# Kernel optimization log

Measured on AMD Instinct MI355X. Metric: run time of the kernel, lower is better.

Reference implementation:

```python
import jax, jax.numpy as jnp
import numpy as np

B, N_E, N_T, N_R, N_W2V = 32, 500000, 2000000, 200, 300


def setup_inputs() -> dict:
    key = jax.random.key(0)
    ks = jax.random.split(key, 11)
    x = jax.random.uniform(ks[0], (B, N_E), dtype=jnp.float32)  # k-hot-like entity vector
    q = jax.random.normal(ks[1], (B, N_W2V), dtype=jnp.float32)
    # Reified KB: one nonzero per row of M_subj / M_rel / M_obj -> index vectors
    subj_idx = jax.random.randint(ks[2], (N_T,), 0, N_E)
    rel_idx = jax.random.randint(ks[3], (N_T,), 0, N_R)
    obj_idx = jax.random.randint(ks[4], (N_T,), 0, N_E)
    s = 1.0 / np.sqrt(N_W2V)
    W1 = jax.random.uniform(ks[5], (N_W2V, N_R), minval=-s, maxval=s, dtype=jnp.float32)
    b1 = jax.random.uniform(ks[6], (N_R,), minval=-s, maxval=s, dtype=jnp.float32)
    W2 = jax.random.uniform(ks[7], (N_W2V, N_R), minval=-s, maxval=s, dtype=jnp.float32)
    b2 = jax.random.uniform(ks[8], (N_R,), minval=-s, maxval=s, dtype=jnp.float32)
    W3 = jax.random.uniform(ks[9], (N_W2V, N_R), minval=-s, maxval=s, dtype=jnp.float32)
    b3 = jax.random.uniform(ks[10], (N_R,), minval=-s, maxval=s, dtype=jnp.float32)
    return {"x": x, "q": q, "subj_idx": subj_idx, "rel_idx": rel_idx,
            "obj_idx": obj_idx, "W1": W1, "b1": b1, "W2": W2, "b2": b2,
            "W3": W3, "b3": b3, "n_hop": 3}


def reference(x, q, subj_idx, rel_idx, obj_idx, W1, b1, W2, b2, W3, b3, n_hop):
    # one follow step: x_t = x @ M_subj.T (gather), r_t = r @ M_rel.T (gather),
    # x_new = (x_t * r_t) @ M_obj (scatter-add over object entities)
    def one_step(x, r):
        m = x[:, subj_idx] * r[:, rel_idx]          # [B, N_T]
        return jnp.zeros_like(x).at[:, obj_idx].add(m)  # [B, N_E]

    if n_hop >= 1:
        x = one_step(x, q @ W1 + b1)
    if n_hop >= 2:
        x = one_step(x, q @ W2 + b2)
    if n_hop >= 3:
        x = one_step(x, q @ W3 + b3)
    return x
```

## Files before the change

### kernel.cpp

```cpp
#include <hip/hip_runtime.h>
#include <hip/hip_fp16.h>

#define B 32
#define NW2V 300
#define NR 200
#define NBLK 256
#define MAXNB 2048
#define CS_THREADS 1024

__global__ void compute_r_kernel(const float* __restrict__ q,
                                 const float* __restrict__ W,
                                 const float* __restrict__ bias,
                                 float* __restrict__ rT) {
    int tid = blockIdx.x * blockDim.x + threadIdx.x;
    if (tid >= NR * B) return;
    int b = tid & (B - 1);
    int j = tid >> 5;
    float acc = bias[j];
    for (int k = 0; k < NW2V; ++k)
        acc += q[b * NW2V + k] * W[k * NR + j];
    rT[j * B + b] = acc;
}

__global__ void transpose_in_kernel(const float* __restrict__ x,
                                    __half* __restrict__ xT, int n_e) {
    __shared__ float tile[64][33];
    int e0 = blockIdx.x * 64;
    for (int p = 0; p < 8; ++p) {
        int idx = p * 256 + threadIdx.x;
        int b = idx >> 6, e = idx & 63;
        if (e0 + e < n_e) tile[e][b] = x[(size_t)b * n_e + e0 + e];
    }
    __syncthreads();
    for (int p = 0; p < 8; ++p) {
        int idx = p * 256 + threadIdx.x;
        int b = idx & 31, e = idx >> 5;
        if (e0 + e < n_e) xT[(size_t)(e0 + e) * B + b] = __float2half(tile[e][b]);
    }
}

__global__ void transpose_out_kernel(const __half* __restrict__ xT,
                                     float* __restrict__ out, int n_e) {
    __shared__ float tile[64][33];
    int e0 = blockIdx.x * 64;
    for (int p = 0; p < 8; ++p) {
        int idx = p * 256 + threadIdx.x;
        int b = idx & 31, e = idx >> 5;
        if (e0 + e < n_e) tile[e][b] = __half2float(xT[(size_t)(e0 + e) * B + b]);
    }
    __syncthreads();
    for (int p = 0; p < 8; ++p) {
        int idx = p * 256 + threadIdx.x;
        int b = idx >> 6, e = idx & 63;
        if (e0 + e < n_e) out[(size_t)b * n_e + e0 + e] = tile[e][b];
    }
}


__global__ void count_kernel(const int* __restrict__ obj,
                             int* __restrict__ hist_bb, int n_t, int nb, int chunk) {
    __shared__ int h[MAXNB];
    for (int i = threadIdx.x; i < nb; i += CS_THREADS) h[i] = 0;
    __syncthreads();
    int t0 = blockIdx.x * chunk;
    int t1 = min(t0 + chunk, n_t);
    for (int t = t0 + threadIdx.x; t < t1; t += CS_THREADS)
        atomicAdd(&h[obj[t] >> 8], 1);
    __syncthreads();
    for (int i = threadIdx.x; i < nb; i += CS_THREADS)
        hist_bb[(size_t)i * NBLK + blockIdx.x] = h[i];
}

__global__ void block_reduce_kernel(const int* __restrict__ vals,
                                    int* __restrict__ blockSums, int len) {
    __shared__ int s[256];
    int i = blockIdx.x * 256 + threadIdx.x;
    s[threadIdx.x] = (i < len) ? vals[i] : 0;
    __syncthreads();
    for (int off = 128; off > 0; off >>= 1) {
        if (threadIdx.x < off) s[threadIdx.x] += s[threadIdx.x + off];
        __syncthreads();
    }
    if (threadIdx.x == 0) blockSums[blockIdx.x] = s[0];
}

__global__ void scan_blocksums_kernel(int* __restrict__ blockSums, int nb) {
    __shared__ int s[256];
    int t = threadIdx.x;
    int local[8];
    int run = 0;
    for (int c = 0; c < 8; ++c) {
        int j = t * 8 + c;
        run += (j < nb) ? blockSums[j] : 0;
        local[c] = run;
    }
    s[t] = run;
    __syncthreads();
    for (int off = 1; off < 256; off <<= 1) {
        int v = (t >= off) ? s[t - off] : 0;
        __syncthreads();
        s[t] += v;
        __syncthreads();
    }
    int threadExcl = s[t] - run;
    for (int c = 0; c < 8; ++c) {
        int j = t * 8 + c;
        if (j < nb) blockSums[j] = threadExcl + (c == 0 ? 0 : local[c - 1]);
    }
}

__global__ void scan_apply_kernel(const int* __restrict__ vals,
                                  const int* __restrict__ blockSums,
                                  int* __restrict__ out, int len) {
    __shared__ int s[256];
    int t = threadIdx.x;
    int i = blockIdx.x * 256 + t;
    int c = (i < len) ? vals[i] : 0;
    s[t] = c;
    __syncthreads();
    for (int off = 1; off < 256; off <<= 1) {
        int v = (t >= off) ? s[t - off] : 0;
        __syncthreads();
        s[t] += v;
        __syncthreads();
    }
    if (i < len) out[i] = blockSums[blockIdx.x] + s[t] - c;
}

__global__ void scatter8_kernel(const int* __restrict__ subj,
                                const int* __restrict__ rel,
                                const int* __restrict__ obj,
                                const int* __restrict__ base_bb,
                                uint2* __restrict__ packed2,
                                int n_t, int nb, int chunk) {
    __shared__ int h[MAXNB];
    __shared__ int sbase[MAXNB];
    for (int i = threadIdx.x; i < nb; i += CS_THREADS) {
        h[i] = 0;
        sbase[i] = base_bb[(size_t)i * NBLK + blockIdx.x];
    }
    __syncthreads();
    int t0 = blockIdx.x * chunk;
    int t1 = min(t0 + chunk, n_t);
    for (int t = t0 + threadIdx.x; t < t1; t += CS_THREADS) {
        int o = obj[t];
        int bin = o >> 8;
        int rank = atomicAdd(&h[bin], 1);
        packed2[sbase[bin] + rank] = make_uint2(
            (unsigned)subj[t] | ((unsigned)rel[t] << 19), (unsigned)o);
    }
}

__global__ void fine_sort_kernel(const uint2* __restrict__ in,
                                 uint2* __restrict__ outp,
                                 const int* __restrict__ base_bb,
                                 int n_t, int nb) {
    __shared__ int cnt[256];
    __shared__ int cur[256];
    int bin = blockIdx.x;
    int beg = base_bb[(size_t)bin * NBLK];
    int end = (bin + 1 < nb) ? base_bb[(size_t)(bin + 1) * NBLK] : n_t;
    int t = threadIdx.x;
    cnt[t] = 0;
    __syncthreads();
    for (int i = beg + t; i < end; i += 256)
        atomicAdd(&cnt[in[i].y & 255], 1);
    __syncthreads();
    int c = cnt[t];
    __syncthreads();
    for (int off = 1; off < 256; off <<= 1) {
        int v = (t >= off) ? cnt[t - off] : 0;
        __syncthreads();
        cnt[t] += v;
        __syncthreads();
    }
    cur[t] = cnt[t] - c + beg;
    __syncthreads();
    for (int i = beg + t; i < end; i += 256) {
        uint2 e = in[i];
        int pos = atomicAdd(&cur[e.y & 255], 1);
        outp[pos] = e;
    }
}

__global__ void hop_merge_kernel(const __half2* __restrict__ xT2,
                                 const float2* __restrict__ rT2,
                                 __half2* __restrict__ outT2,
                                 const uint2* __restrict__ sorted2,
                                 const int* __restrict__ n_hop,
                                 int hop, int n_e, int n_t) {
    int tid = threadIdx.x;
    if (*n_hop < hop) {
        long total = (long)n_e * 16;
        for (long i = (long)blockIdx.x * 256 + tid; i < total;
             i += (long)gridDim.x * 256)
            outT2[i] = xT2[i];
        return;
    }
    __shared__ uint2 ent[256];
    int base = blockIdx.x * 256;
    int cnt = min(256, n_t - base);
    ent[tid] = (tid < cnt) ? sorted2[base + tid]
                           : make_uint2(0u, 0xFFFFFFFFu);
    __syncthreads();
    int g = tid >> 4, l = tid & 15;
    int e0 = g * 16;
    int m = min(16, cnt - e0);
    if (m <= 0) return;

    __half2 xh[16];
#pragma unroll
    for (int j = 0; j < 16; ++j) {
        int s = (int)(ent[e0 + j].x & 0x7FFFF);
        xh[j] = xT2[(size_t)s * 16 + l];
    }

    float a0 = 0.f, a1 = 0.f;
    unsigned cur_o = ent[e0].y;
#pragma unroll
    for (int j = 0; j < 16; ++j) {
        if (j < m) {
            uint2 e = ent[e0 + j];
            float2 rf = rT2[(size_t)(e.x >> 19) * 16 + l];
            float2 xf = __half22float2(xh[j]);
            if (e.y != cur_o) {
                unsafeAtomicAdd(&outT2[(size_t)cur_o * 16 + l],
                                __floats2half2_rn(a0, a1));
                a0 = 0.f; a1 = 0.f;
                cur_o = e.y;
            }
            a0 += xf.x * rf.x;
            a1 += xf.y * rf.y;
        }
    }
    unsafeAtomicAdd(&outT2[(size_t)cur_o * 16 + l], __floats2half2_rn(a0, a1));
}

extern "C" void kernel_launch(void* const* d_in, const int* in_sizes, int n_in,
                              void* d_out, int out_size, void* d_ws, size_t ws_size,
                              hipStream_t stream) {
    const float* x    = (const float*)d_in[0];
    const float* q    = (const float*)d_in[1];
    const int*   subj = (const int*)d_in[2];
    const int*   rel  = (const int*)d_in[3];
    const int*   obj  = (const int*)d_in[4];
    const float* W1   = (const float*)d_in[5];
    const float* bb1  = (const float*)d_in[6];
    const float* W2   = (const float*)d_in[7];
    const float* bb2  = (const float*)d_in[8];
    const float* W3   = (const float*)d_in[9];
    const float* bb3  = (const float*)d_in[10];
    const int*   n_hop = (const int*)d_in[11];
    float* out = (float*)d_out;

    const int n_e   = in_sizes[0] / B;
    const int n_t   = in_sizes[2];
    const int nb    = (n_e + 255) >> 8;
    const int chunk = (n_t + NBLK - 1) / NBLK;
    const int scanLen = nb * NBLK;
    const int snb   = (scanLen + 255) / 256;

    char* w = (char*)d_ws;
    __half* bufA    = (__half*)w;                     w += 32000000;
    __half* bufB    = (__half*)w;                     w += 32000000;
    float*  rT      = (float*)w;                      w += 76800;
    int*    hist_bb = (int*)w;                        w += 2097152;
    int*    base_bb = (int*)w;                        w += 2097152;
    int*    bsums   = (int*)w;                        w += 16384;
    uint2*  packed2 = (uint2*)w;                      w += 16000000;
    uint2*  sorted2 = (uint2*)w;

    const int rblocks = (NR * B + 255) / 256;
    compute_r_kernel<<<rblocks, 256, 0, stream>>>(q, W1, bb1, rT + 0 * NR * B);
    compute_r_kernel<<<rblocks, 256, 0, stream>>>(q, W2, bb2, rT + 1 * NR * B);
    compute_r_kernel<<<rblocks, 256, 0, stream>>>(q, W3, bb3, rT + 2 * NR * B);

    const int tblocks = (n_e + 63) / 64;
    transpose_in_kernel<<<tblocks, 256, 0, stream>>>(x, bufA, n_e);

    count_kernel<<<NBLK, CS_THREADS, 0, stream>>>(obj, hist_bb, n_t, nb, chunk);
    block_reduce_kernel<<<snb, 256, 0, stream>>>(hist_bb, bsums, scanLen);
    scan_blocksums_kernel<<<1, 256, 0, stream>>>(bsums, snb);
    scan_apply_kernel<<<snb, 256, 0, stream>>>(hist_bb, bsums, base_bb, scanLen);
    scatter8_kernel<<<NBLK, CS_THREADS, 0, stream>>>(subj, rel, obj, base_bb,
                                                     packed2, n_t, nb, chunk);
    fine_sort_kernel<<<nb, 256, 0, stream>>>(packed2, sorted2, base_bb, n_t, nb);

    const int hblocks = (n_t + 255) / 256;
    const size_t bytes = (size_t)n_e * B * sizeof(__half);

    hipMemsetAsync(bufB, 0, bytes, stream);
    hop_merge_kernel<<<hblocks, 256, 0, stream>>>((const __half2*)bufA,
        (const float2*)(rT + 0 * NR * B), (__half2*)bufB, sorted2, n_hop, 1, n_e, n_t);
    hipMemsetAsync(bufA, 0, bytes, stream);
    hop_merge_kernel<<<hblocks, 256, 0, stream>>>((const __half2*)bufB,
        (const float2*)(rT + 1 * NR * B), (__half2*)bufA, sorted2, n_hop, 2, n_e, n_t);
    hipMemsetAsync(bufB, 0, bytes, stream);
    hop_merge_kernel<<<hblocks, 256, 0, stream>>>((const __half2*)bufA,
        (const float2*)(rT + 2 * NR * B), (__half2*)bufB, sorted2, n_hop, 3, n_e, n_t);

    transpose_out_kernel<<<tblocks, 256, 0, stream>>>(bufB, out, n_e);
}
```

Measured before the change: 336.4 us.

## Accumulate each object bucket in shared memory instead of global half2 atomics

Each hop kernel now runs one block per 256-entity object bucket. The block walks that bucket's sorted triples and accumulates into an fp32 shared-memory tile with LDS atomics, then writes the tile to the output once. This drops the three hipMemsetAsync zeroing passes and the global half2 atomics, and keeps accumulation in fp32 until the final store. In exchange each block loops serially over its bucket, about 1000 triples, and needs roughly 35KB of LDS per block, which may limit occupancy.

```diff
diff --git a/kernel.cpp b/kernel.cpp
--- a/kernel.cpp
+++ b/kernel.cpp
@@ -183,57 +183,78 @@
     }
 }
 
-__global__ void hop_merge_kernel(const __half2* __restrict__ xT2,
-                                 const float2* __restrict__ rT2,
-                                 __half2* __restrict__ outT2,
-                                 const uint2* __restrict__ sorted2,
-                                 const int* __restrict__ n_hop,
-                                 int hop, int n_e, int n_t) {
+__global__ void hop_bucket_kernel(const __half2* __restrict__ xT2,
+                                  const float2* __restrict__ rT2,
+                                  __half2* __restrict__ outT2,
+                                  const uint2* __restrict__ sorted2,
+                                  const int* __restrict__ base_bb,
+                                  const int* __restrict__ n_hop,
+                                  int hop, int n_e, int n_t, int nb) {
     int tid = threadIdx.x;
+    int bin = blockIdx.x;
+    int eb = bin << 8;
+    int lim = min(256, n_e - eb);
+
     if (*n_hop < hop) {
-        long total = (long)n_e * 16;
-        for (long i = (long)blockIdx.x * 256 + tid; i < total;
-             i += (long)gridDim.x * 256)
-            outT2[i] = xT2[i];
+        for (int p = tid; p < lim * 16; p += 256)
+            outT2[(size_t)eb * 16 + p] = xT2[(size_t)eb * 16 + p];
         return;
     }
+
+    __shared__ float acc[256][33];
     __shared__ uint2 ent[256];
-    int base = blockIdx.x * 256;
-    int cnt = min(256, n_t - base);
-    ent[tid] = (tid < cnt) ? sorted2[base + tid]
-                           : make_uint2(0u, 0xFFFFFFFFu);
-    __syncthreads();
+    float* af = &acc[0][0];
+    for (int i = tid; i < 256 * 33; i += 256) af[i] = 0.f;
+
+    int beg = base_bb[(size_t)bin * NBLK];
+    int end = (bin + 1 < nb) ? base_bb[(size_t)(bin + 1) * NBLK] : n_t;
     int g = tid >> 4, l = tid & 15;
     int e0 = g * 16;
-    int m = min(16, cnt - e0);
-    if (m <= 0) return;
-
-    __half2 xh[16];
+
+    for (int c0 = beg; c0 < end; c0 += 256) {
+        int cnt = min(256, end - c0);
+        __syncthreads();
+        ent[tid] = (tid < cnt) ? sorted2[c0 + tid]
+                               : make_uint2(0u, 0xFFFFFFFFu);
+        __syncthreads();
+        int m = min(16, cnt - e0);
+        if (m > 0) {
+            __half2 xh[16];
 #pragma unroll
-    for (int j = 0; j < 16; ++j) {
-        int s = (int)(ent[e0 + j].x & 0x7FFFF);
-        xh[j] = xT2[(size_t)s * 16 + l];
-    }
-
-    float a0 = 0.f, a1 = 0.f;
-    unsigned cur_o = ent[e0].y;
+            for (int j = 0; j < 16; ++j) {
+                int s = (int)(ent[e0 + j].x & 0x7FFFF);
+                xh[j] = xT2[(size_t)s * 16 + l];
+            }
+            float a0 = 0.f, a1 = 0.f;
+            unsigned cur_o = ent[e0].y;
 #pragma unroll
-    for (int j = 0; j < 16; ++j) {
-        if (j < m) {
-            uint2 e = ent[e0 + j];
-            float2 rf = rT2[(size_t)(e.x >> 19) * 16 + l];
-            float2 xf = __half22float2(xh[j]);
-            if (e.y != cur_o) {
-                unsafeAtomicAdd(&outT2[(size_t)cur_o * 16 + l],
-                                __floats2half2_rn(a0, a1));
-                a0 = 0.f; a1 = 0.f;
-                cur_o = e.y;
+            for (int j = 0; j < 16; ++j) {
+                if (j < m) {
+                    uint2 e = ent[e0 + j];
+                    float2 rf = rT2[(size_t)(e.x >> 19) * 16 + l];
+                    float2 xf = __half22float2(xh[j]);
+                    if (e.y != cur_o) {
+                        int le = (int)(cur_o & 255);
+                        atomicAdd(&acc[le][2 * l], a0);
+                        atomicAdd(&acc[le][2 * l + 1], a1);
+                        a0 = 0.f; a1 = 0.f;
+                        cur_o = e.y;
+                    }
+                    a0 += xf.x * rf.x;
+                    a1 += xf.y * rf.y;
+                }
             }
-            a0 += xf.x * rf.x;
-            a1 += xf.y * rf.y;
+            int le = (int)(cur_o & 255);
+            atomicAdd(&acc[le][2 * l], a0);
+            atomicAdd(&acc[le][2 * l + 1], a1);
         }
     }
-    unsafeAtomicAdd(&outT2[(size_t)cur_o * 16 + l], __floats2half2_rn(a0, a1));
+    __syncthreads();
+    for (int p = tid; p < lim * 16; p += 256) {
+        int e = p >> 4, lw = p & 15;
+        outT2[(size_t)(eb + e) * 16 + lw] =
+            __floats2half2_rn(acc[e][2 * lw], acc[e][2 * lw + 1]);
+    }
 }
 
 extern "C" void kernel_launch(void* const* d_in, const int* in_sizes, int n_in,
@@ -286,18 +307,15 @@
                                                      packed2, n_t, nb, chunk);
     fine_sort_kernel<<<nb, 256, 0, stream>>>(packed2, sorted2, base_bb, n_t, nb);
 
-    const int hblocks = (n_t + 255) / 256;
-    const size_t bytes = (size_t)n_e * B * sizeof(__half);
-
-    hipMemsetAsync(bufB, 0, bytes, stream);
-    hop_merge_kernel<<<hblocks, 256, 0, stream>>>((const __half2*)bufA,
-        (const float2*)(rT + 0 * NR * B), (__half2*)bufB, sorted2, n_hop, 1, n_e, n_t);
-    hipMemsetAsync(bufA, 0, bytes, stream);
-    hop_merge_kernel<<<hblocks, 256, 0, stream>>>((const __half2*)bufB,
-        (const float2*)(rT + 1 * NR * B), (__half2*)bufA, sorted2, n_hop, 2, n_e, n_t);
-    hipMemsetAsync(bufB, 0, bytes, stream);
-    hop_merge_kernel<<<hblocks, 256, 0, stream>>>((const __half2*)bufA,
-        (const float2*)(rT + 2 * NR * B), (__half2*)bufB, sorted2, n_hop, 3, n_e, n_t);
+    hop_bucket_kernel<<<nb, 256, 0, stream>>>((const __half2*)bufA,
+        (const float2*)(rT + 0 * NR * B), (__half2*)bufB, sorted2, base_bb,
+        n_hop, 1, n_e, n_t, nb);
+    hop_bucket_kernel<<<nb, 256, 0, stream>>>((const __half2*)bufB,
+        (const float2*)(rT + 1 * NR * B), (__half2*)bufA, sorted2, base_bb,
+        n_hop, 2, n_e, n_t, nb);
+    hop_bucket_kernel<<<nb, 256, 0, stream>>>((const __half2*)bufA,
+        (const float2*)(rT + 2 * NR * B), (__half2*)bufB, sorted2, base_bb,
+        n_hop, 3, n_e, n_t, nb);
 
     transpose_out_kernel<<<tblocks, 256, 0, stream>>>(bufB, out, n_e);
 }
```

Result: slower. 502.9 us (+49.5%).

## Sort triples by subject partition then object, and partition hop blocks by subject range

Applied to the files above, without the earlier changes.

The coarse bin key becomes a combination of the subject's top bits (8 partitions of 65536 entities) and the object's high bits. Fine sort now works on 2048 sub-bins per coarse bin, with a two-level local scan. Each hop kernel block is assigned to one subject partition via blockIdx&7 and grid-strides over that partition's sorted segment. The aim is to improve cache locality of the x gathers, since each partition touches only a ~4MB slice of x. In exchange, runs of equal object are split across partitions, which adds atomics, and the sort kernels carry larger histograms and extra scan work. It also assumes n_e fits the hardcoded bit split.

```diff
diff --git a/kernel.cpp b/kernel.cpp
--- a/kernel.cpp
+++ b/kernel.cpp
@@ -5,8 +5,11 @@
 #define NW2V 300
 #define NR 200
 #define NBLK 256
+#define NB_C 2048
 #define MAXNB 2048
 #define CS_THREADS 1024
+#define HOP_PB 1024
+
 
 __global__ void compute_r_kernel(const float* __restrict__ q,
                                  const float* __restrict__ W,
@@ -57,17 +60,20 @@
 }
 
 
-__global__ void count_kernel(const int* __restrict__ obj,
-                             int* __restrict__ hist_bb, int n_t, int nb, int chunk) {
+__global__ void count_kernel(const int* __restrict__ subj,
+                             const int* __restrict__ obj,
+                             int* __restrict__ hist_bb, int n_t, int chunk) {
     __shared__ int h[MAXNB];
-    for (int i = threadIdx.x; i < nb; i += CS_THREADS) h[i] = 0;
+    for (int i = threadIdx.x; i < NB_C; i += CS_THREADS) h[i] = 0;
     __syncthreads();
     int t0 = blockIdx.x * chunk;
     int t1 = min(t0 + chunk, n_t);
-    for (int t = t0 + threadIdx.x; t < t1; t += CS_THREADS)
-        atomicAdd(&h[obj[t] >> 8], 1);
-    __syncthreads();
-    for (int i = threadIdx.x; i < nb; i += CS_THREADS)
+    for (int t = t0 + threadIdx.x; t < t1; t += CS_THREADS) {
+        int bin = ((subj[t] >> 16) << 8) | (obj[t] >> 11);
+        atomicAdd(&h[bin], 1);
+    }
+    __syncthreads();
+    for (int i = threadIdx.x; i < NB_C; i += CS_THREADS)
         hist_bb[(size_t)i * NBLK + blockIdx.x] = h[i];
 }
 
@@ -132,10 +138,10 @@
                                 const int* __restrict__ obj,
                                 const int* __restrict__ base_bb,
                                 uint2* __restrict__ packed2,
-                                int n_t, int nb, int chunk) {
+                                int n_t, int chunk) {
     __shared__ int h[MAXNB];
     __shared__ int sbase[MAXNB];
-    for (int i = threadIdx.x; i < nb; i += CS_THREADS) {
+    for (int i = threadIdx.x; i < NB_C; i += CS_THREADS) {
         h[i] = 0;
         sbase[i] = base_bb[(size_t)i * NBLK + blockIdx.x];
     }
@@ -144,7 +150,7 @@
     int t1 = min(t0 + chunk, n_t);
     for (int t = t0 + threadIdx.x; t < t1; t += CS_THREADS) {
         int o = obj[t];
-        int bin = o >> 8;
+        int bin = ((subj[t] >> 16) << 8) | (o >> 11);
         int rank = atomicAdd(&h[bin], 1);
         packed2[sbase[bin] + rank] = make_uint2(
             (unsigned)subj[t] | ((unsigned)rel[t] << 19), (unsigned)o);
@@ -154,31 +160,37 @@
 __global__ void fine_sort_kernel(const uint2* __restrict__ in,
                                  uint2* __restrict__ outp,
                                  const int* __restrict__ base_bb,
-                                 int n_t, int nb) {
-    __shared__ int cnt[256];
-    __shared__ int cur[256];
+                                 int n_t) {
+    __shared__ int cnt[2048];
+    __shared__ int cur[2048];
+    __shared__ int ts[256];
     int bin = blockIdx.x;
     int beg = base_bb[(size_t)bin * NBLK];
-    int end = (bin + 1 < nb) ? base_bb[(size_t)(bin + 1) * NBLK] : n_t;
+    int end = (bin + 1 < NB_C) ? base_bb[(size_t)(bin + 1) * NBLK] : n_t;
     int t = threadIdx.x;
-    cnt[t] = 0;
+    for (int k = t; k < 2048; k += 256) cnt[k] = 0;
     __syncthreads();
     for (int i = beg + t; i < end; i += 256)
-        atomicAdd(&cnt[in[i].y & 255], 1);
-    __syncthreads();
-    int c = cnt[t];
+        atomicAdd(&cnt[in[i].y & 2047], 1);
+    __syncthreads();
+    int loc[8];
+    int run = 0;
+    for (int c = 0; c < 8; ++c) { run += cnt[t * 8 + c]; loc[c] = run; }
+    ts[t] = run;
     __syncthreads();
     for (int off = 1; off < 256; off <<= 1) {
-        int v = (t >= off) ? cnt[t - off] : 0;
-        __syncthreads();
-        cnt[t] += v;
-        __syncthreads();
-    }
-    cur[t] = cnt[t] - c + beg;
+        int v = (t >= off) ? ts[t - off] : 0;
+        __syncthreads();
+        ts[t] += v;
+        __syncthreads();
+    }
+    int excl = ts[t] - run;
+    for (int c = 0; c < 8; ++c)
+        cur[t * 8 + c] = beg + excl + (c == 0 ? 0 : loc[c - 1]);
     __syncthreads();
     for (int i = beg + t; i < end; i += 256) {
         uint2 e = in[i];
-        int pos = atomicAdd(&cur[e.y & 255], 1);
+        int pos = atomicAdd(&cur[e.y & 2047], 1);
         outp[pos] = e;
     }
 }
@@ -187,6 +199,7 @@
                                  const float2* __restrict__ rT2,
                                  __half2* __restrict__ outT2,
                                  const uint2* __restrict__ sorted2,
+                                 const int* __restrict__ base_bb,
                                  const int* __restrict__ n_hop,
                                  int hop, int n_e, int n_t) {
     int tid = threadIdx.x;
@@ -197,43 +210,51 @@
             outT2[i] = xT2[i];
         return;
     }
+    int p = blockIdx.x & 7;
+    int ib = blockIdx.x >> 3;
+    int pbeg = base_bb[(size_t)(p << 8) * NBLK];
+    int pend = (p == 7) ? n_t : base_bb[(size_t)((p + 1) << 8) * NBLK];
+
     __shared__ uint2 ent[256];
-    int base = blockIdx.x * 256;
-    int cnt = min(256, n_t - base);
-    ent[tid] = (tid < cnt) ? sorted2[base + tid]
-                           : make_uint2(0u, 0xFFFFFFFFu);
-    __syncthreads();
     int g = tid >> 4, l = tid & 15;
     int e0 = g * 16;
-    int m = min(16, cnt - e0);
-    if (m <= 0) return;
-
-    __half2 xh[16];
+
+    for (int base = pbeg + (ib << 8); base < pend; base += (HOP_PB << 8)) {
+        int cnt = min(256, pend - base);
+        __syncthreads();
+        ent[tid] = (tid < cnt) ? sorted2[base + tid]
+                               : make_uint2(0u, 0xFFFFFFFFu);
+        __syncthreads();
+        int m = min(16, cnt - e0);
+        if (m > 0) {
+            __half2 xh[16];
 #pragma unroll
-    for (int j = 0; j < 16; ++j) {
-        int s = (int)(ent[e0 + j].x & 0x7FFFF);
-        xh[j] = xT2[(size_t)s * 16 + l];
-    }
-
-    float a0 = 0.f, a1 = 0.f;
-    unsigned cur_o = ent[e0].y;
+            for (int j = 0; j < 16; ++j) {
+                int s = (int)(ent[e0 + j].x & 0x7FFFF);
+                xh[j] = xT2[(size_t)s * 16 + l];
+            }
+            float a0 = 0.f, a1 = 0.f;
+            unsigned cur_o = ent[e0].y;
 #pragma unroll
-    for (int j = 0; j < 16; ++j) {
-        if (j < m) {
-            uint2 e = ent[e0 + j];
-            float2 rf = rT2[(size_t)(e.x >> 19) * 16 + l];
-            float2 xf = __half22float2(xh[j]);
-            if (e.y != cur_o) {
-                unsafeAtomicAdd(&outT2[(size_t)cur_o * 16 + l],
-                                __floats2half2_rn(a0, a1));
-                a0 = 0.f; a1 = 0.f;
-                cur_o = e.y;
+            for (int j = 0; j < 16; ++j) {
+                if (j < m) {
+                    uint2 e = ent[e0 + j];
+                    float2 rf = rT2[(size_t)(e.x >> 19) * 16 + l];
+                    float2 xf = __half22float2(xh[j]);
+                    if (e.y != cur_o) {
+                        unsafeAtomicAdd(&outT2[(size_t)cur_o * 16 + l],
+                                        __floats2half2_rn(a0, a1));
+                        a0 = 0.f; a1 = 0.f;
+                        cur_o = e.y;
+                    }
+                    a0 += xf.x * rf.x;
+                    a1 += xf.y * rf.y;
+                }
             }
-            a0 += xf.x * rf.x;
-            a1 += xf.y * rf.y;
+            unsafeAtomicAdd(&outT2[(size_t)cur_o * 16 + l],
+                            __floats2half2_rn(a0, a1));
         }
     }
-    unsafeAtomicAdd(&outT2[(size_t)cur_o * 16 + l], __floats2half2_rn(a0, a1));
 }
 
 extern "C" void kernel_launch(void* const* d_in, const int* in_sizes, int n_in,
@@ -255,9 +276,8 @@
 
     const int n_e   = in_sizes[0] / B;
     const int n_t   = in_sizes[2];
-    const int nb    = (n_e + 255) >> 8;
     const int chunk = (n_t + NBLK - 1) / NBLK;
-    const int scanLen = nb * NBLK;
+    const int scanLen = NB_C * NBLK;
     const int snb   = (scanLen + 255) / 256;
 
     char* w = (char*)d_ws;
@@ -278,26 +298,29 @@
     const int tblocks = (n_e + 63) / 64;
     transpose_in_kernel<<<tblocks, 256, 0, stream>>>(x, bufA, n_e);
 
-    count_kernel<<<NBLK, CS_THREADS, 0, stream>>>(obj, hist_bb, n_t, nb, chunk);
+    count_kernel<<<NBLK, CS_THREADS, 0, stream>>>(subj, obj, hist_bb, n_t, chunk);
     block_reduce_kernel<<<snb, 256, 0, stream>>>(hist_bb, bsums, scanLen);
     scan_blocksums_kernel<<<1, 256, 0, stream>>>(bsums, snb);
     scan_apply_kernel<<<snb, 256, 0, stream>>>(hist_bb, bsums, base_bb, scanLen);
     scatter8_kernel<<<NBLK, CS_THREADS, 0, stream>>>(subj, rel, obj, base_bb,
-                                                     packed2, n_t, nb, chunk);
-    fine_sort_kernel<<<nb, 256, 0, stream>>>(packed2, sorted2, base_bb, n_t, nb);
-
-    const int hblocks = (n_t + 255) / 256;
+                                                     packed2, n_t, chunk);
+    fine_sort_kernel<<<NB_C, 256, 0, stream>>>(packed2, sorted2, base_bb, n_t);
+
+    const int hblocks = 8 * HOP_PB;
     const size_t bytes = (size_t)n_e * B * sizeof(__half);
 
     hipMemsetAsync(bufB, 0, bytes, stream);
     hop_merge_kernel<<<hblocks, 256, 0, stream>>>((const __half2*)bufA,
-        (const float2*)(rT + 0 * NR * B), (__half2*)bufB, sorted2, n_hop, 1, n_e, n_t);
+        (const float2*)(rT + 0 * NR * B), (__half2*)bufB, sorted2, base_bb,
+        n_hop, 1, n_e, n_t);
     hipMemsetAsync(bufA, 0, bytes, stream);
     hop_merge_kernel<<<hblocks, 256, 0, stream>>>((const __half2*)bufB,
-        (const float2*)(rT + 1 * NR * B), (__half2*)bufA, sorted2, n_hop, 2, n_e, n_t);
+        (const float2*)(rT + 1 * NR * B), (__half2*)bufA, sorted2, base_bb,
+        n_hop, 2, n_e, n_t);
     hipMemsetAsync(bufB, 0, bytes, stream);
     hop_merge_kernel<<<hblocks, 256, 0, stream>>>((const __half2*)bufA,
-        (const float2*)(rT + 2 * NR * B), (__half2*)bufB, sorted2, n_hop, 3, n_e, n_t);
+        (const float2*)(rT + 2 * NR * B), (__half2*)bufB, sorted2, base_bb,
+        n_hop, 3, n_e, n_t);
 
     transpose_out_kernel<<<tblocks, 256, 0, stream>>>(bufB, out, n_e);
 }
```

New measurement: 467.2 us. +38.9%, slower.
